# Optimization experiments

Hardware: AMD Instinct MI355X
Metric: run time of the kernel (lower is better)

The kernel has to match this reference:

```python
import jax, jax.numpy as jnp
import numpy as np

# dims: N patches, D_IN input feats, D model, DI=inner, DS=state, DC=conv, DTR=dt_rank
N, D_IN, D, DI, DS, DC, DTR, NC, NL = 4096, 1024, 512, 1024, 16, 4, 32, 4, 2


def setup_inputs() -> dict:
    key = jax.random.key(0)
    ks = jax.random.split(key, 16)
    g = lambda i, shape, s=0.02: jax.random.normal(ks[i], shape, dtype=jnp.float32) * s
    return {
        "data_s": jax.random.normal(ks[0], (N, 512), dtype=jnp.float32),
        "data_l": jax.random.normal(ks[1], (N, 512), dtype=jnp.float32),
        "coord_s": jax.random.uniform(ks[2], (N, 2), dtype=jnp.float32) * 1000.0,
        "label": jax.random.randint(ks[3], (1,), 0, NC),
        "fc1_w": g(4, (D, D_IN)), "fc1_b": jnp.zeros((D,), jnp.float32),
        "ln_w": jnp.ones((NL, D), jnp.float32), "ln_b": jnp.zeros((NL, D), jnp.float32),
        "in_proj_w": g(5, (NL, 2 * DI, D)),
        "conv_w": g(6, (NL, DI, DC), 0.1), "conv_b": jnp.zeros((NL, DI), jnp.float32),
        "x_proj_w": g(7, (NL, DTR + 2 * DS, DI)),
        "dt_proj_w": g(8, (NL, DI, DTR), 0.1), "dt_proj_b": g(9, (NL, DI), 0.5),
        "A_log": jnp.broadcast_to(jnp.log(jnp.arange(1, DS + 1, dtype=jnp.float32)), (NL, DI, DS)) + jnp.zeros((NL, DI, DS), jnp.float32),
        "D_param": jnp.ones((NL, DI), jnp.float32),
        "out_proj_w": g(10, (NL, D, DI)),
        "norm_w": jnp.ones((D,), jnp.float32), "norm_b": jnp.zeros((D,), jnp.float32),
        "attn_w1": g(11, (128, D)), "attn_b1": jnp.zeros((128,), jnp.float32),
        "attn_w2": g(12, (1, 128)), "attn_b2": jnp.zeros((1,), jnp.float32),
        "cls_w": g(13, (NC, D)), "cls_b": jnp.zeros((NC,), jnp.float32),
    }


def _layer_norm(x, w, b, eps=1e-5):
    m = x.mean(-1, keepdims=True)
    v = ((x - m) ** 2).mean(-1, keepdims=True)
    return (x - m) * jax.lax.rsqrt(v + eps) * w + b


def _mamba(h, inw, cw, cb, xpw, dtw, dtb, Alog, Dp, ow):
    # h: (B, L, D) -> (B, L, D); canonical Mamba block (mamba_ssm defaults)
    B, L, _ = h.shape
    xz = h @ inw.T                      # (B, L, 2*DI)
    x, z = jnp.split(xz, 2, axis=-1)
    # causal depthwise conv1d, kernel DC, left pad DC-1 (== torch pad+truncate)
    xp = jnp.pad(x, ((0, 0), (DC - 1, 0), (0, 0)))
    x = sum(xp[:, k:k + L, :] * cw[:, k] for k in range(DC)) + cb
    x = jax.nn.silu(x)
    xdbl = x @ xpw.T                    # (B, L, DTR + 2*DS)
    dt, Bm, Cm = jnp.split(xdbl, [DTR, DTR + DS], axis=-1)
    dt = jax.nn.softplus(dt @ dtw.T + dtb)   # (B, L, DI)
    A = -jnp.exp(Alog)                  # (DI, DS)
    dA = jnp.exp(dt[..., None] * A)                          # (B, L, DI, DS)
    dBx = dt[..., None] * Bm[:, :, None, :] * x[..., None]   # (B, L, DI, DS)

    def step(hst, inp):
        dA_t, dBx_t, C_t = inp
        hst = dA_t * hst + dBx_t        # (B, DI, DS)
        return hst, jnp.einsum('bds,bs->bd', hst, C_t)

    h0 = jnp.zeros((B, DI, DS), x.dtype)
    _, ys = jax.lax.scan(step, h0, (jnp.swapaxes(dA, 0, 1), jnp.swapaxes(dBx, 0, 1), jnp.swapaxes(Cm, 0, 1)))
    y = jnp.swapaxes(ys, 0, 1) + Dp * x
    return (y * jax.nn.silu(z)) @ ow.T


def _forward(data_s, data_l, coord_s, fc1_w, fc1_b, ln_w, ln_b, in_proj_w, conv_w, conv_b,
             x_proj_w, dt_proj_w, dt_proj_b, A_log, D_param, out_proj_w, norm_w, norm_b,
             attn_w1, attn_b1, attn_w2, attn_b2, cls_w, cls_b, label):
    h = jnp.concatenate([data_s, data_l], axis=1)            # (N, 1024)
    packed = jnp.concatenate([h, coord_s], axis=1)[None]     # (1, N, 1026)
    h = packed[:, :, :-2]                                    # strip coords
    h = jax.nn.relu(h @ fc1_w.T + fc1_b)                     # dropout: eval mode (identity)
    for i in range(NL):
        res = h
        hn = _layer_norm(h, ln_w[i], ln_b[i])
        h = _mamba(hn, in_proj_w[i], conv_w[i], conv_b[i], x_proj_w[i], dt_proj_w[i],
                   dt_proj_b[i], A_log[i], D_param[i], out_proj_w[i]) + res
    h = _layer_norm(h, norm_w, norm_b)
    A = jnp.tanh(h @ attn_w1.T + attn_b1) @ attn_w2.T + attn_b2   # (1, N, 1)
    A = jax.nn.softmax(jnp.swapaxes(A, 1, 2), axis=-1)            # (1, 1, N)
    hp = (A @ h)[0]                                               # (1, D)
    logits = hp @ cls_w.T + cls_b                                 # (1, NC)
    hz = jax.nn.sigmoid(logits)
    p = jnp.clip(hz, 1e-6, 1.0 - 1e-6)
    lce = jnp.log(p) - jnp.log1p(-p)                              # torch.logit
    Y_prob = jax.nn.softmax(lce, axis=1)
    loss = -jnp.take(jax.nn.log_softmax(lce, axis=1)[0], label[0])
    return lce, Y_prob, loss


def reference(data_s, data_l, coord_s, label, fc1_w, fc1_b, ln_w, ln_b, in_proj_w, conv_w,
              conv_b, x_proj_w, dt_proj_w, dt_proj_b, A_log, D_param, out_proj_w, norm_w,
              norm_b, attn_w1, attn_b1, attn_w2, attn_b2, cls_w, cls_b):
    return _forward(data_s, data_l, coord_s, fc1_w, fc1_b, ln_w, ln_b, in_proj_w, conv_w,
                    conv_b, x_proj_w, dt_proj_w, dt_proj_b, A_log, D_param, out_proj_w,
                    norm_w, norm_b, attn_w1, attn_b1, attn_w2, attn_b2, cls_w, cls_b, label)
```

## Files before the change

### kernel.cpp

```cpp
#include <hip/hip_runtime.h>
#include <math.h>

#define L_SEQ 4096
#define DMODEL 512
#define DIN    1024
#define DI     1024
#define DS     16
#define DC     4
#define DTR    32
#define NCHK   512
#define CL     8
#define SLAB   (L_SEQ * 64)

typedef __bf16 bf16x8 __attribute__((ext_vector_type(8)));
typedef __bf16 bf16x4 __attribute__((ext_vector_type(4)));
typedef float floatx4 __attribute__((ext_vector_type(4)));

#define RLN2 1.44269504f
#define LN2  0.69314718f

__device__ __forceinline__ float softplus_fast(float x) {
    if (x > 20.f) return x;
    float e = __builtin_amdgcn_exp2f(x * RLN2);
    return LN2 * __builtin_amdgcn_logf(1.f + e);
}

__device__ __forceinline__ void gl2lds16(const __bf16* g, __bf16* l) {
    __builtin_amdgcn_global_load_lds(
        (const __attribute__((address_space(1))) void*)g,
        (__attribute__((address_space(3))) void*)l, 16, 0, 0);
}

template <int BN, int ACT, bool BIAS, bool ADDDEST, bool OUTBF, int KS>
__global__ __launch_bounds__(256) void gemm_mfma(
    const __bf16* __restrict__ A, int lda,
    const __bf16* __restrict__ W, int ldw,
    const float* __restrict__ bias,
    float* __restrict__ C, __bf16* __restrict__ Cb, int ldc, int K)
{
    __shared__ __align__(16) __bf16 sA[128 * 32];
    __shared__ __align__(16) __bf16 sB[BN * 32];
    const int tid = threadIdx.x;
    const int wid = tid >> 6, lane = tid & 63;
    const int m0 = blockIdx.y * 128;
    int n0;
    if (KS > 1) {
        const int ksl = blockIdx.x;
        A += (size_t)ksl * K;
        W += (size_t)ksl * K;
        C += (size_t)ksl * (size_t)gridDim.y * 128 * ldc;
        n0 = 0;
    } else {
        n0 = blockIdx.x * BN;
    }

    constexpr int MR = (BN == 128) ? 4 : 2;
    constexpr int NR = 4;
    const int wrow = (BN == 128) ? (wid >> 1) * 64 : wid * 32;
    const int wcol = (BN == 128) ? (wid & 1) * 64 : 0;

    const int srowA0 = wid * 32 + (lane >> 2);
    const int scol   = (lane & 3) * 8;
    const __bf16* aSrc0 = A + (size_t)(m0 + srowA0) * lda + scol;
    const __bf16* aSrc1 = aSrc0 + 16 * (size_t)lda;
    __bf16* aDst0 = &sA[wid * 1024];
    __bf16* aDst1 = &sA[wid * 1024 + 512];

    const __bf16* bSrc0;
    const __bf16* bSrc1 = nullptr;
    __bf16* bDst0;
    __bf16* bDst1 = nullptr;
    if (BN == 128) {
        bSrc0 = W + (size_t)(n0 + wid * 32 + (lane >> 2)) * ldw + scol;
        bSrc1 = bSrc0 + 16 * (size_t)ldw;
        bDst0 = &sB[wid * 1024];
        bDst1 = &sB[wid * 1024 + 512];
    } else {
        bSrc0 = W + (size_t)(n0 + wid * 16 + (lane >> 2)) * ldw + scol;
        bDst0 = &sB[wid * 512];
    }

    floatx4 acc[MR][NR] = {};
    const int fr = lane & 15;
    const int fk = (lane >> 4) * 8;

    for (int k0 = 0; k0 < K; k0 += 32) {
        __syncthreads();
        gl2lds16(aSrc0 + k0, aDst0);
        gl2lds16(aSrc1 + k0, aDst1);
        gl2lds16(bSrc0 + k0, bDst0);
        if (BN == 128) gl2lds16(bSrc1 + k0, bDst1);
        __syncthreads();
        bf16x8 af[MR], bfv[NR];
#pragma unroll
        for (int i = 0; i < MR; ++i)
            af[i] = *(const bf16x8*)&sA[(wrow + i * 16 + fr) * 32 + fk];
#pragma unroll
        for (int j = 0; j < NR; ++j)
            bfv[j] = *(const bf16x8*)&sB[(wcol + j * 16 + fr) * 32 + fk];
#pragma unroll
        for (int i = 0; i < MR; ++i)
#pragma unroll
            for (int j = 0; j < NR; ++j)
                acc[i][j] = __builtin_amdgcn_mfma_f32_16x16x32_bf16(
                    af[i], bfv[j], acc[i][j], 0, 0, 0);
    }

#pragma unroll
    for (int i = 0; i < MR; ++i)
#pragma unroll
        for (int j = 0; j < NR; ++j) {
            const int n = n0 + wcol + j * 16 + fr;
            float bv = 0.f;
            if (BIAS) bv = bias[n];
#pragma unroll
            for (int r = 0; r < 4; ++r) {
                const int m = m0 + wrow + i * 16 + (lane >> 4) * 4 + r;
                float v = acc[i][j][r] + bv;
                if (ACT == 1) v = fmaxf(v, 0.f);
                else if (ACT == 2) v = tanhf(v);
                const size_t idx = (size_t)m * ldc + n;
                if (OUTBF) {
                    Cb[idx] = (__bf16)v;
                } else {
                    if (ADDDEST) v += C[idx];
                    C[idx] = v;
                }
            }
        }
}

__global__ void prep_k(const float* __restrict__ s0, __bf16* __restrict__ d0, int n0,
                       const float* __restrict__ s1, __bf16* __restrict__ d1, int n1,
                       const float* __restrict__ s2, __bf16* __restrict__ d2, int n2,
                       const float* __restrict__ s3, __bf16* __restrict__ d3, int n3,
                       const float* __restrict__ s4, __bf16* __restrict__ d4, int n4,
                       const float* __restrict__ dtw, float* __restrict__ dtwT, int n5)
{
    int i = blockIdx.x * 256 + threadIdx.x;
    int tot = n0 + n1 + n2 + n3 + n4;
    if (i >= tot) {
        int j = i - tot;
        if (j < n5) {
            int l = j >> 15, rem = j & 32767, r = rem >> 5, k = rem & 31;
            dtwT[l * 32768 + k * 1024 + r] = dtw[j];
        }
        return;
    }
    const float* s; __bf16* d; int base;
    if (i < n0) { s = s0; d = d0; base = i; }
    else if (i < n0 + n1) { s = s1; d = d1; base = i - n0; }
    else if (i < n0 + n1 + n2) { s = s2; d = d2; base = i - n0 - n1; }
    else if (i < n0 + n1 + n2 + n3) { s = s3; d = d3; base = i - n0 - n1 - n2; }
    else { s = s4; d = d4; base = i - n0 - n1 - n2 - n3; }
    float4 a = ((const float4*)s)[2 * base], b = ((const float4*)s)[2 * base + 1];
    bf16x8 v;
    v[0] = (__bf16)a.x; v[1] = (__bf16)a.y; v[2] = (__bf16)a.z; v[3] = (__bf16)a.w;
    v[4] = (__bf16)b.x; v[5] = (__bf16)b.y; v[6] = (__bf16)b.z; v[7] = (__bf16)b.w;
    *(bf16x8*)&d[8 * base] = v;
}

__global__ void concat_bf_k(const float* __restrict__ a,
                            const float* __restrict__ b,
                            __bf16* __restrict__ o)
{
    int idx = blockIdx.x * 256 + threadIdx.x;
    int m = idx >> 7, c8 = (idx & 127) << 3;
    const float* src = (c8 < 512) ? &a[(m << 9) + c8] : &b[(m << 9) + c8 - 512];
    float4 x = ((const float4*)src)[0], y = ((const float4*)src)[1];
    bf16x8 v;
    v[0] = (__bf16)x.x; v[1] = (__bf16)x.y; v[2] = (__bf16)x.z; v[3] = (__bf16)x.w;
    v[4] = (__bf16)y.x; v[5] = (__bf16)y.y; v[6] = (__bf16)y.z; v[7] = (__bf16)y.w;
    *(bf16x8*)&o[idx << 3] = v;
}

template <int OMODE>
__global__ __launch_bounds__(128) void layernorm_k(
    const float* __restrict__ X, const float* __restrict__ w,
    const float* __restrict__ b, float* __restrict__ Yf, __bf16* __restrict__ Yb)
{
    const int r = blockIdx.x, tid = threadIdx.x;
    const size_t base = ((size_t)r << 9) + (tid << 2);
    const float4 v = *(const float4*)&X[base];
    float s = v.x + v.y + v.z + v.w;
#pragma unroll
    for (int o = 32; o; o >>= 1) s += __shfl_down(s, o, 64);
    __shared__ float red[2];
    if ((tid & 63) == 0) red[tid >> 6] = s;
    __syncthreads();
    const float mean = (red[0] + red[1]) * (1.f / 512.f);
    float dx = v.x - mean, dy = v.y - mean, dz = v.z - mean, dw = v.w - mean;
    float q = dx * dx + dy * dy + dz * dz + dw * dw;
#pragma unroll
    for (int o = 32; o; o >>= 1) q += __shfl_down(q, o, 64);
    __shared__ float red2[2];
    if ((tid & 63) == 0) red2[tid >> 6] = q;
    __syncthreads();
    const float rs = rsqrtf((red2[0] + red2[1]) * (1.f / 512.f) + 1e-5f);
    const float4 wv = *(const float4*)&w[tid << 2];
    const float4 bv = *(const float4*)&b[tid << 2];
    float o0 = dx * rs * wv.x + bv.x;
    float o1 = dy * rs * wv.y + bv.y;
    float o2 = dz * rs * wv.z + bv.z;
    float o3 = dw * rs * wv.w + bv.w;
    if (OMODE != 1) {
        float4 ov; ov.x = o0; ov.y = o1; ov.z = o2; ov.w = o3;
        *(float4*)&Yf[base] = ov;
    }
    if (OMODE != 0) {
        bf16x4 ov; ov[0] = (__bf16)o0; ov[1] = (__bf16)o1;
        ov[2] = (__bf16)o2; ov[3] = (__bf16)o3;
        *(bf16x4*)&Yb[base] = ov;
    }
}

__global__ void conv_silu_k(const __bf16* __restrict__ XZb,
                            const float* __restrict__ cw,
                            const float* __restrict__ cb,
                            __bf16* __restrict__ XCb)
{
    int i = blockIdx.x * 256 + threadIdx.x;
    int t = i >> 8, d4 = (i & 255) << 2;
    float wt[4][4];
#pragma unroll
    for (int d = 0; d < 4; ++d) {
        float4 w = *(const float4*)&cw[(d4 + d) << 2];
        wt[d][0] = w.x; wt[d][1] = w.y; wt[d][2] = w.z; wt[d][3] = w.w;
    }
    float4 c = *(const float4*)&cb[d4];
    float a0 = c.x, a1 = c.y, a2 = c.z, a3 = c.w;
#pragma unroll
    for (int k = 0; k < 4; ++k) {
        int ts = t + k - 3;
        if (ts >= 0) {
            bf16x4 x = *(const bf16x4*)&XZb[((size_t)ts << 11) + d4];
            a0 = fmaf((float)x[0], wt[0][k], a0);
            a1 = fmaf((float)x[1], wt[1][k], a1);
            a2 = fmaf((float)x[2], wt[2][k], a2);
            a3 = fmaf((float)x[3], wt[3][k], a3);
        }
    }
    a0 *= 1.f / (1.f + __expf(-a0));
    a1 *= 1.f / (1.f + __expf(-a1));
    a2 *= 1.f / (1.f + __expf(-a2));
    a3 *= 1.f / (1.f + __expf(-a3));
    bf16x4 ob; ob[0] = (__bf16)a0; ob[1] = (__bf16)a1;
    ob[2] = (__bf16)a2; ob[3] = (__bf16)a3;
    *(bf16x4*)&XCb[((size_t)t << 10) + d4] = ob;
}

__global__ __launch_bounds__(256) void scanA_k(
    const __bf16* __restrict__ xc, const float* __restrict__ xdblP,
    const float* __restrict__ dtwT, const float* __restrict__ dtb,
    const float* __restrict__ Alog,
    __bf16* __restrict__ sP, __bf16* __restrict__ sH,
    __bf16* __restrict__ dtg)
{
    const int d = blockIdx.x * 256 + threadIdx.x;
    const int c = blockIdx.y;
    const int tid = threadIdx.x;
    __shared__ float xlow[CL][DTR];
    __shared__ float Bs[CL][DS];
    __shared__ float dts[CL][256];
    {
        int t = tid >> 5, k = tid & 31;
        size_t g = (size_t)(c * CL + t) * 64 + k;
        xlow[t][k] = xdblP[g] + xdblP[SLAB + g] + xdblP[2 * SLAB + g] + xdblP[3 * SLAB + g];
    }
    if (tid < CL * DS) {
        int t = tid >> 4, s = tid & 15;
        size_t g = (size_t)(c * CL + t) * 64 + 32 + s;
        Bs[t][s] = xdblP[g] + xdblP[SLAB + g] + xdblP[2 * SLAB + g] + xdblP[3 * SLAB + g];
    }
    __syncthreads();
    float dtw_d[32];
#pragma unroll
    for (int k = 0; k < 32; ++k) dtw_d[k] = dtwT[k * 1024 + d];
    const float dtb_d = dtb[d];
    float sumdt = 0.f;
#pragma unroll
    for (int t = 0; t < CL; ++t) {
        float p0 = 0.f, p1 = 0.f, p2 = 0.f, p3 = 0.f;
#pragma unroll
        for (int k4 = 0; k4 < 8; ++k4) {
            float4 xq = *(const float4*)&xlow[t][k4 * 4];
            p0 = fmaf(xq.x, dtw_d[k4 * 4 + 0], p0);
            p1 = fmaf(xq.y, dtw_d[k4 * 4 + 1], p1);
            p2 = fmaf(xq.z, dtw_d[k4 * 4 + 2], p2);
            p3 = fmaf(xq.w, dtw_d[k4 * 4 + 3], p3);
        }
        float acc = ((p0 + p1) + (p2 + p3)) + dtb_d;
        float dtv = softplus_fast(acc);
        dts[t][tid] = dtv;
        dtg[((size_t)(c * CL + t) << 10) + d] = (__bf16)dtv;
        sumdt += dtv;
    }
    float As2[DS], h[DS];
    {
        const float4* Ap4 = (const float4*)&Alog[(size_t)d * DS];
#pragma unroll
        for (int q = 0; q < 4; ++q) {
            float4 a = Ap4[q];
            As2[q * 4 + 0] = -__expf(a.x) * RLN2; As2[q * 4 + 1] = -__expf(a.y) * RLN2;
            As2[q * 4 + 2] = -__expf(a.z) * RLN2; As2[q * 4 + 3] = -__expf(a.w) * RLN2;
        }
    }
#pragma unroll
    for (int s = 0; s < DS; ++s) h[s] = 0.f;
    for (int t = 0; t < CL; ++t) {
        float dtv = dts[t][tid];
        float xv = (float)xc[((size_t)(c * CL + t) << 10) + d];
        float dx = dtv * xv;
        float barr[16];
#pragma unroll
        for (int q = 0; q < 4; ++q) {
            float4 b = *(const float4*)&Bs[t][q * 4];
            barr[q * 4 + 0] = b.x; barr[q * 4 + 1] = b.y;
            barr[q * 4 + 2] = b.z; barr[q * 4 + 3] = b.w;
        }
#pragma unroll
        for (int s = 0; s < DS; ++s) {
            float a = exp2f(dtv * As2[s]);
            h[s] = fmaf(a, h[s], dx * barr[s]);
        }
    }
    size_t base = ((size_t)c * DI + d) * DS;
    bf16x8 p0v, p1v, h0v, h1v;
#pragma unroll
    for (int s = 0; s < 8; ++s) {
        p0v[s] = (__bf16)exp2f(As2[s] * sumdt);
        p1v[s] = (__bf16)exp2f(As2[s + 8] * sumdt);
        h0v[s] = (__bf16)h[s];
        h1v[s] = (__bf16)h[s + 8];
    }
    *(bf16x8*)&sP[base] = p0v; *(bf16x8*)&sP[base + 8] = p1v;
    *(bf16x8*)&sH[base] = h0v; *(bf16x8*)&sH[base + 8] = h1v;
}

__global__ __launch_bounds__(64) void scanB_k(
    const __bf16* __restrict__ sP, const __bf16* __restrict__ sH,
    __bf16* __restrict__ Hin)
{
    int p = blockIdx.x * 64 + threadIdx.x;
    float run = 0.f;
#pragma unroll 4
    for (int c = 0; c < NCHK; ++c) {
        size_t idx = (size_t)c * DI * DS + p;
        Hin[idx] = (__bf16)run;
        run = fmaf((float)sP[idx], run, (float)sH[idx]);
    }
}

__global__ __launch_bounds__(256) void scanC_k(
    const __bf16* __restrict__ xc, const float* __restrict__ xdblP,
    const __bf16* __restrict__ dtg,
    const float* __restrict__ Alog, const float* __restrict__ Dp,
    const __bf16* __restrict__ XZb, const __bf16* __restrict__ Hin,
    __bf16* __restrict__ yz)
{
    const int d = blockIdx.x * 256 + threadIdx.x;
    const int c = blockIdx.y;
    const int tid = threadIdx.x;
    __shared__ float Bs[CL][DS], Cs[CL][DS];
    if (tid < CL * DS) {
        int t = tid >> 4, s = tid & 15;
        size_t g = (size_t)(c * CL + t) * 64 + 32 + s;
        Bs[t][s] = xdblP[g] + xdblP[SLAB + g] + xdblP[2 * SLAB + g] + xdblP[3 * SLAB + g];
        g += 16;
        Cs[t][s] = xdblP[g] + xdblP[SLAB + g] + xdblP[2 * SLAB + g] + xdblP[3 * SLAB + g];
    }
    __syncthreads();
    float As2[DS], h[DS];
    {
        const float4* Ap4 = (const float4*)&Alog[(size_t)d * DS];
#pragma unroll
        for (int q = 0; q < 4; ++q) {
            float4 a = Ap4[q];
            As2[q * 4 + 0] = -__expf(a.x) * RLN2; As2[q * 4 + 1] = -__expf(a.y) * RLN2;
            As2[q * 4 + 2] = -__expf(a.z) * RLN2; As2[q * 4 + 3] = -__expf(a.w) * RLN2;
        }
    }
    {
        size_t base = ((size_t)c * DI + d) * DS;
        bf16x8 h0 = *(const bf16x8*)&Hin[base];
        bf16x8 h1 = *(const bf16x8*)&Hin[base + 8];
#pragma unroll
        for (int s = 0; s < 8; ++s) { h[s] = (float)h0[s]; h[s + 8] = (float)h1[s]; }
    }
    const float Dd = Dp[d];
    for (int t = 0; t < CL; ++t) {
        size_t tg = (size_t)(c * CL + t);
        const float dtv = (float)dtg[(tg << 10) + d];
        const float xv = (float)xc[(tg << 10) + d];
        const float dx = dtv * xv;
        float barr[16], carr[16];
#pragma unroll
        for (int q = 0; q < 4; ++q) {
            float4 b = *(const float4*)&Bs[t][q * 4];
            float4 cc = *(const float4*)&Cs[t][q * 4];
            barr[q * 4 + 0] = b.x; barr[q * 4 + 1] = b.y;
            barr[q * 4 + 2] = b.z; barr[q * 4 + 3] = b.w;
            carr[q * 4 + 0] = cc.x; carr[q * 4 + 1] = cc.y;
            carr[q * 4 + 2] = cc.z; carr[q * 4 + 3] = cc.w;
        }
        float y = 0.f;
#pragma unroll
        for (int s = 0; s < DS; ++s) {
            float a = exp2f(dtv * As2[s]);
            h[s] = fmaf(a, h[s], dx * barr[s]);
            y = fmaf(h[s], carr[s], y);
        }
        y = fmaf(Dd, xv, y);
        float zv = (float)XZb[(tg << 11) + 1024 + d];
        float sg = 1.f / (1.f + __expf(-zv));
        yz[(tg << 10) + d] = (__bf16)(y * (zv * sg));
    }
}

__global__ void score_k(const float* __restrict__ At,
                        const float* __restrict__ w2,
                        const float* __restrict__ b2,
                        float* __restrict__ sc)
{
    int t = blockIdx.x * 256 + threadIdx.x;
    const float4* a = (const float4*)(At + ((size_t)t << 7));
    const float4* w = (const float4*)w2;
    float acc = 0.f;
#pragma unroll
    for (int j = 0; j < 32; ++j) {
        float4 av = a[j], wv = w[j];
        acc += av.x * wv.x + av.y * wv.y + av.z * wv.z + av.w * wv.w;
    }
    sc[t] = acc + b2[0];
}

__global__ __launch_bounds__(256) void softmax_k(const float* __restrict__ s,
                                                 float* __restrict__ p)
{
    const int tid = threadIdx.x;
    float vals[16];
#pragma unroll
    for (int i = 0; i < 4; ++i) {
        float4 v = *(const float4*)&s[(tid << 4) + (i << 2)];
        vals[i * 4 + 0] = v.x; vals[i * 4 + 1] = v.y;
        vals[i * 4 + 2] = v.z; vals[i * 4 + 3] = v.w;
    }
    float mx = -1e30f;
#pragma unroll
    for (int i = 0; i < 16; ++i) mx = fmaxf(mx, vals[i]);
#pragma unroll
    for (int o = 32; o; o >>= 1) mx = fmaxf(mx, __shfl_xor(mx, o, 64));
    __shared__ float red[4];
    if ((tid & 63) == 0) red[tid >> 6] = mx;
    __syncthreads();
    mx = fmaxf(fmaxf(red[0], red[1]), fmaxf(red[2], red[3]));
    float sum = 0.f, e[16];
#pragma unroll
    for (int i = 0; i < 16; ++i) { e[i] = __expf(vals[i] - mx); sum += e[i]; }
#pragma unroll
    for (int o = 32; o; o >>= 1) sum += __shfl_xor(sum, o, 64);
    __syncthreads();
    if ((tid & 63) == 0) red[tid >> 6] = sum;
    __syncthreads();
    sum = red[0] + red[1] + red[2] + red[3];
    float inv = 1.f / sum;
#pragma unroll
    for (int i = 0; i < 4; ++i) {
        float4 ov;
        ov.x = e[i * 4 + 0] * inv; ov.y = e[i * 4 + 1] * inv;
        ov.z = e[i * 4 + 2] * inv; ov.w = e[i * 4 + 3] * inv;
        *(float4*)&p[(tid << 4) + (i << 2)] = ov;
    }
}

__global__ void pool_partial_k(const float* __restrict__ prob,
                               const float* __restrict__ hln,
                               float* __restrict__ part)
{
    int j = blockIdx.x * 256 + threadIdx.x;
    int c = blockIdx.y;
    float acc = 0.f;
    for (int t = c * 128; t < (c + 1) * 128; ++t)
        acc = fmaf(prob[t], hln[((size_t)t << 9) + j], acc);
    part[c * 512 + j] = acc;
}

__global__ void pool_reduce_k(const float* __restrict__ part,
                              float* __restrict__ hp)
{
    int j = blockIdx.x * 256 + threadIdx.x;
    float acc = 0.f;
    for (int c = 0; c < 32; ++c) acc += part[c * 512 + j];
    hp[j] = acc;
}

__global__ __launch_bounds__(256) void final_head_k(
    const float* __restrict__ hp, const float* __restrict__ cls_w,
    const float* __restrict__ cls_b, const int* __restrict__ label,
    float* __restrict__ out)
{
    const int w = threadIdx.x >> 6, lane = threadIdx.x & 63;
    float acc = 0.f;
    for (int k = lane; k < 512; k += 64) acc += hp[k] * cls_w[w * 512 + k];
#pragma unroll
    for (int o = 32; o; o >>= 1) acc += __shfl_down(acc, o, 64);
    __shared__ float lg[4];
    if (lane == 0) lg[w] = acc + cls_b[w];
    __syncthreads();
    if (threadIdx.x == 0) {
        float lce[4];
        for (int c = 0; c < 4; ++c) {
            float z = lg[c];
            float hz = 1.f / (1.f + expf(-z));
            float pc = fminf(fmaxf(hz, 1e-6f), 1.f - 1e-6f);
            lce[c] = logf(pc) - log1pf(-pc);
        }
        float mx = fmaxf(fmaxf(lce[0], lce[1]), fmaxf(lce[2], lce[3]));
        float se = 0.f;
        for (int c = 0; c < 4; ++c) se += expf(lce[c] - mx);
        for (int c = 0; c < 4; ++c) out[c] = lce[c];
        for (int c = 0; c < 4; ++c) out[4 + c] = expf(lce[c] - mx) / se;
        int lb = label[0];
        out[8] = -(lce[lb] - mx - logf(se));
    }
}

extern "C" void kernel_launch(void* const* d_in, const int* in_sizes, int n_in,
                              void* d_out, int out_size, void* d_ws, size_t ws_size,
                              hipStream_t stream)
{
    const float* data_s   = (const float*)d_in[0];
    const float* data_l   = (const float*)d_in[1];
    const int*   label    = (const int*)d_in[3];
    const float* fc1_w    = (const float*)d_in[4];
    const float* fc1_b    = (const float*)d_in[5];
    const float* ln_w     = (const float*)d_in[6];
    const float* ln_b     = (const float*)d_in[7];
    const float* in_proj_w= (const float*)d_in[8];
    const float* conv_w   = (const float*)d_in[9];
    const float* conv_b   = (const float*)d_in[10];
    const float* x_proj_w = (const float*)d_in[11];
    const float* dt_proj_w= (const float*)d_in[12];
    const float* dt_proj_b= (const float*)d_in[13];
    const float* A_log    = (const float*)d_in[14];
    const float* D_param  = (const float*)d_in[15];
    const float* out_proj_w=(const float*)d_in[16];
    const float* norm_w   = (const float*)d_in[17];
    const float* norm_b   = (const float*)d_in[18];
    const float* attn_w1  = (const float*)d_in[19];
    const float* attn_b1  = (const float*)d_in[20];
    const float* attn_w2  = (const float*)d_in[21];
    const float* attn_b2  = (const float*)d_in[22];
    const float* cls_w    = (const float*)d_in[23];
    const float* cls_b    = (const float*)d_in[24];
    float* out = (float*)d_out;

    float* ws = (float*)d_ws;
    size_t off = 0;
    float* h     = ws + off; off += (size_t)L_SEQ * DMODEL;
    float* hn    = ws + off; off += (size_t)L_SEQ * DMODEL;
    float* xdblP = ws + off; off += (size_t)4 * SLAB;
    float* dtwT  = ws + off; off += (size_t)2 * DTR * DI;
    float* At    = ws + off; off += (size_t)L_SEQ * 128;
    float* sc    = ws + off; off += L_SEQ;
    float* pb    = ws + off; off += L_SEQ;
    float* part  = ws + off; off += 32 * 512;
    float* hp    = ws + off; off += 512;

    __bf16* bws = (__bf16*)(ws + off);
    size_t boff = 0;
    __bf16* Acatb = bws + boff; boff += (size_t)L_SEQ * DIN;
    __bf16* hnb   = bws + boff; boff += (size_t)L_SEQ * DMODEL;
    __bf16* XZb   = bws + boff; boff += (size_t)L_SEQ * 2 * DI;
    __bf16* XCb   = bws + boff; boff += (size_t)L_SEQ * DI;
    __bf16* yzb   = bws + boff; boff += (size_t)L_SEQ * DI;
    __bf16* sPb   = bws + boff; boff += (size_t)NCHK * DI * DS;
    __bf16* sHb   = bws + boff; boff += (size_t)NCHK * DI * DS;
    __bf16* HinB  = bws + boff; boff += (size_t)NCHK * DI * DS;
    __bf16* dtgB  = bws + boff; boff += (size_t)L_SEQ * DI;
    __bf16* wfc1b = bws + boff; boff += (size_t)DMODEL * DIN;
    __bf16* winb  = bws + boff; boff += (size_t)2 * 2 * DI * DMODEL;
    __bf16* wxpb  = bws + boff; boff += (size_t)2 * 64 * DI;
    __bf16* woutb = bws + boff; boff += (size_t)2 * DMODEL * DI;
    __bf16* w1b   = bws + boff; boff += (size_t)128 * DMODEL;
    if (ws_size < off * sizeof(float) + boff * sizeof(__bf16)) return;

    const int n0 = DMODEL * DIN / 8;
    const int n1 = 2 * 2 * DI * DMODEL / 8;
    const int n2 = 2 * 64 * DI / 8;
    const int n3 = 2 * DMODEL * DI / 8;
    const int n4 = 128 * DMODEL / 8;
    const int n5 = 2 * DI * DTR;
    prep_k<<<(n0 + n1 + n2 + n3 + n4 + n5 + 255) / 256, 256, 0, stream>>>(
        fc1_w, wfc1b, n0, in_proj_w, winb, n1, x_proj_w, wxpb, n2,
        out_proj_w, woutb, n3, attn_w1, w1b, n4, dt_proj_w, dtwT, n5);

    concat_bf_k<<<L_SEQ * DIN / 8 / 256, 256, 0, stream>>>(data_s, data_l, Acatb);
    gemm_mfma<64, 1, true, false, false, 1><<<dim3(DMODEL / 64, L_SEQ / 128), 256, 0, stream>>>(
        Acatb, DIN, wfc1b, DIN, fc1_b, h, nullptr, DMODEL, DIN);

    for (int i = 0; i < 2; ++i) {
        const __bf16* inw = winb + (size_t)i * 2 * DI * DMODEL;
        const float* cwi = conv_w + (size_t)i * DI * DC;
        const float* cbi = conv_b + (size_t)i * DI;
        const __bf16* xpw = wxpb + (size_t)i * 64 * DI;
        const float* dtwTi = dtwT + (size_t)i * DTR * DI;
        const float* dtbv= dt_proj_b + (size_t)i * DI;
        const float* Alg = A_log + (size_t)i * DI * DS;
        const float* Dpi = D_param + (size_t)i * DI;
        const __bf16* owi = woutb + (size_t)i * DMODEL * DI;

        layernorm_k<1><<<L_SEQ, 128, 0, stream>>>(h, ln_w + i * DMODEL, ln_b + i * DMODEL, nullptr, hnb);
        gemm_mfma<128, 0, false, false, true, 1><<<dim3(2 * DI / 128, L_SEQ / 128), 256, 0, stream>>>(
            hnb, DMODEL, inw, DMODEL, nullptr, nullptr, XZb, 2 * DI, DMODEL);
        conv_silu_k<<<L_SEQ * DI / 4 / 256, 256, 0, stream>>>(XZb, cwi, cbi, XCb);
        gemm_mfma<64, 0, false, false, false, 4><<<dim3(4, L_SEQ / 128), 256, 0, stream>>>(
            XCb, DI, xpw, DI, nullptr, xdblP, nullptr, 64, DI / 4);
        scanA_k<<<dim3(DI / 256, NCHK), 256, 0, stream>>>(XCb, xdblP, dtwTi, dtbv, Alg, sPb, sHb, dtgB);
        scanB_k<<<DI * DS / 64, 64, 0, stream>>>(sPb, sHb, HinB);
        scanC_k<<<dim3(DI / 256, NCHK), 256, 0, stream>>>(XCb, xdblP, dtgB, Alg, Dpi, XZb, HinB, yzb);
        gemm_mfma<64, 0, false, true, false, 1><<<dim3(DMODEL / 64, L_SEQ / 128), 256, 0, stream>>>(
            yzb, DI, owi, DI, nullptr, h, nullptr, DMODEL, DI);
    }

    layernorm_k<2><<<L_SEQ, 128, 0, stream>>>(h, norm_w, norm_b, hn, hnb);
    gemm_mfma<64, 2, true, false, false, 1><<<dim3(2, L_SEQ / 128), 256, 0, stream>>>(
        hnb, DMODEL, w1b, DMODEL, attn_b1, At, nullptr, 128, DMODEL);
    score_k<<<L_SEQ / 256, 256, 0, stream>>>(At, attn_w2, attn_b2, sc);
    softmax_k<<<1, 256, 0, stream>>>(sc, pb);
    pool_partial_k<<<dim3(2, 32), 256, 0, stream>>>(pb, hn, part);
    pool_reduce_k<<<2, 256, 0, stream>>>(part, hp);
    final_head_k<<<1, 256, 0, stream>>>(hp, cls_w, cls_b, label, out);
}
```

Measured before the change: 449.1 us.

## Split sequential chunk-state scan into hierarchical three-pass group scan

Replaces the single serial 512-step inter-chunk scan with a three-pass scan: per-group reductions of decay products and states over 32 groups of 16 chunks, a short 32-step scan over group aggregates, then a per-group apply pass. This multiplies the number of parallel blocks to hide memory latency of the long dependent chain. It rereads sP/sH twice and stores group products in bf16, adding traffic and slight rounding differences.

```diff
diff --git a/kernel.cpp b/kernel.cpp
--- a/kernel.cpp
+++ b/kernel.cpp
@@ -10,6 +10,9 @@
 #define DTR    32
 #define NCHK   512
 #define CL     8
+#define NPAIR  (DI * DS)
+#define NG     32
+#define GS     16
 #define SLAB   (L_SEQ * 64)
 
 typedef __bf16 bf16x8 __attribute__((ext_vector_type(8)));
@@ -337,15 +340,48 @@
     *(bf16x8*)&sH[base] = h0v; *(bf16x8*)&sH[base + 8] = h1v;
 }
 
-__global__ __launch_bounds__(64) void scanB_k(
+__global__ __launch_bounds__(256) void scanB1_k(
     const __bf16* __restrict__ sP, const __bf16* __restrict__ sH,
-    __bf16* __restrict__ Hin)
-{
-    int p = blockIdx.x * 64 + threadIdx.x;
+    __bf16* __restrict__ PG, __bf16* __restrict__ HG)
+{
+    int p = blockIdx.x * 256 + threadIdx.x;
+    int g = blockIdx.y;
+    float rp = 1.f, rh = 0.f;
+#pragma unroll
+    for (int k = 0; k < GS; ++k) {
+        size_t idx = (size_t)(g * GS + k) * NPAIR + p;
+        float P = (float)sP[idx], H = (float)sH[idx];
+        rh = fmaf(P, rh, H);
+        rp *= P;
+    }
+    PG[(size_t)g * NPAIR + p] = (__bf16)rp;
+    HG[(size_t)g * NPAIR + p] = (__bf16)rh;
+}
+
+__global__ __launch_bounds__(256) void scanB2_k(
+    const __bf16* __restrict__ PG, const __bf16* __restrict__ HG,
+    __bf16* __restrict__ Gin)
+{
+    int p = blockIdx.x * 256 + threadIdx.x;
     float run = 0.f;
-#pragma unroll 4
-    for (int c = 0; c < NCHK; ++c) {
-        size_t idx = (size_t)c * DI * DS + p;
+#pragma unroll
+    for (int g = 0; g < NG; ++g) {
+        size_t idx = (size_t)g * NPAIR + p;
+        Gin[idx] = (__bf16)run;
+        run = fmaf((float)PG[idx], run, (float)HG[idx]);
+    }
+}
+
+__global__ __launch_bounds__(256) void scanB3_k(
+    const __bf16* __restrict__ sP, const __bf16* __restrict__ sH,
+    const __bf16* __restrict__ Gin, __bf16* __restrict__ Hin)
+{
+    int p = blockIdx.x * 256 + threadIdx.x;
+    int g = blockIdx.y;
+    float run = (float)Gin[(size_t)g * NPAIR + p];
+#pragma unroll
+    for (int k = 0; k < GS; ++k) {
+        size_t idx = (size_t)(g * GS + k) * NPAIR + p;
         Hin[idx] = (__bf16)run;
         run = fmaf((float)sP[idx], run, (float)sH[idx]);
     }
@@ -574,10 +610,13 @@
     __bf16* XZb   = bws + boff; boff += (size_t)L_SEQ * 2 * DI;
     __bf16* XCb   = bws + boff; boff += (size_t)L_SEQ * DI;
     __bf16* yzb   = bws + boff; boff += (size_t)L_SEQ * DI;
-    __bf16* sPb   = bws + boff; boff += (size_t)NCHK * DI * DS;
-    __bf16* sHb   = bws + boff; boff += (size_t)NCHK * DI * DS;
-    __bf16* HinB  = bws + boff; boff += (size_t)NCHK * DI * DS;
+    __bf16* sPb   = bws + boff; boff += (size_t)NCHK * NPAIR;
+    __bf16* sHb   = bws + boff; boff += (size_t)NCHK * NPAIR;
+    __bf16* HinB  = bws + boff; boff += (size_t)NCHK * NPAIR;
     __bf16* dtgB  = bws + boff; boff += (size_t)L_SEQ * DI;
+    __bf16* PGb   = bws + boff; boff += (size_t)NG * NPAIR;
+    __bf16* HGb   = bws + boff; boff += (size_t)NG * NPAIR;
+    __bf16* GinB  = bws + boff; boff += (size_t)NG * NPAIR;
     __bf16* wfc1b = bws + boff; boff += (size_t)DMODEL * DIN;
     __bf16* winb  = bws + boff; boff += (size_t)2 * 2 * DI * DMODEL;
     __bf16* wxpb  = bws + boff; boff += (size_t)2 * 64 * DI;
@@ -617,7 +656,9 @@
         gemm_mfma<64, 0, false, false, false, 4><<<dim3(4, L_SEQ / 128), 256, 0, stream>>>(
             XCb, DI, xpw, DI, nullptr, xdblP, nullptr, 64, DI / 4);
         scanA_k<<<dim3(DI / 256, NCHK), 256, 0, stream>>>(XCb, xdblP, dtwTi, dtbv, Alg, sPb, sHb, dtgB);
-        scanB_k<<<DI * DS / 64, 64, 0, stream>>>(sPb, sHb, HinB);
+        scanB1_k<<<dim3(NPAIR / 256, NG), 256, 0, stream>>>(sPb, sHb, PGb, HGb);
+        scanB2_k<<<NPAIR / 256, 256, 0, stream>>>(PGb, HGb, GinB);
+        scanB3_k<<<dim3(NPAIR / 256, NG), 256, 0, stream>>>(sPb, sHb, GinB, HinB);
         scanC_k<<<dim3(DI / 256, NCHK), 256, 0, stream>>>(XCb, xdblP, dtgB, Alg, Dpi, XZb, HinB, yzb);
         gemm_mfma<64, 0, false, true, false, 1><<<dim3(DMODEL / 64, L_SEQ / 128), 256, 0, stream>>>(
             yzb, DI, owi, DI, nullptr, h, nullptr, DMODEL, DI);
```

After: 393.9 us, median of 2. 12.3% less time.
